# Kernel tuning notes

Measured on AMD Instinct MI355X. Metric: run time of the kernel, lower is better.

The kernel has to match this reference:

```python
import jax, jax.numpy as jnp
import numpy as np

N_ENTITIES = 200000
N_EDGES = 1200000
N_RELATIONS = 32
LATDIM = 64
N_HOPS = 2
RES_LAMBDA = 0.5  # args.res_lambda
LEAKY_SLOPE = 0.2
EPS = 1e-12


def setup_inputs() -> dict:
    key = jax.random.key(0)
    k1, k2, k3, k4, k5 = jax.random.split(key, 5)
    entity_emb = jax.random.normal(k1, (N_ENTITIES, LATDIM), dtype=jnp.float32)
    relation_emb = jax.random.normal(k2, (N_RELATIONS, LATDIM), dtype=jnp.float32)
    W = jax.random.normal(k3, (2 * LATDIM, LATDIM), dtype=jnp.float32) * (1.0 / np.sqrt(2 * LATDIM))
    edge_index = jax.random.randint(k4, (2, N_EDGES), 0, N_ENTITIES, dtype=jnp.int64)
    edge_type = jax.random.randint(k5, (N_EDGES,), 0, N_RELATIONS, dtype=jnp.int64)
    return {"entity_emb": entity_emb, "relation_emb": relation_emb, "W": W,
            "edge_index": edge_index, "edge_type": edge_type}


def _l2_normalize(x):
    # F.normalize(x) : row-wise L2 normalize with eps clamp
    n = jnp.sqrt(jnp.sum(x * x, axis=-1, keepdims=True))
    return x / jnp.maximum(n, EPS)


def _agg(entity_emb, relation_emb, W, head, tail, edge_type):
    n = entity_emb.shape[0]
    # gather head/tail embeddings -> [E, 2*D]
    a_input = jnp.concatenate([entity_emb[head], entity_emb[tail]], axis=-1)
    # attention logit per edge: ((a_input @ W) * r_e).sum(-1)
    e = jnp.sum((a_input @ W) * relation_emb[edge_type], axis=-1)
    e = jax.nn.leaky_relu(e, LEAKY_SLOPE)
    # scatter_softmax over edges grouped by head node
    m = jax.ops.segment_max(e, head, num_segments=n)
    ex = jnp.exp(e - m[head])
    denom = jax.ops.segment_sum(ex, head, num_segments=n)
    alpha = ex / denom[head]
    # scatter_sum of alpha-weighted tail embeddings
    agg_emb = jax.ops.segment_sum(entity_emb[tail] * alpha[:, None], head, num_segments=n)
    return agg_emb + entity_emb


def reference(entity_emb, relation_emb, W, edge_index, edge_type):
    head, tail = edge_index[0], edge_index[1]
    entity_res_emb = entity_emb
    ent = entity_emb
    for _ in range(N_HOPS):
        ent = _agg(ent, relation_emb, W, head, tail, edge_type)
        ent = _l2_normalize(ent)  # mess_dropout disabled (deterministic reference)
        entity_res_emb = RES_LAMBDA * entity_res_emb + ent
    return entity_res_emb
```

## Files before the change

kernel.cpp:

```cpp
#include <hip/hip_runtime.h>
#include <hip/hip_bf16.h>


#define N_ENT  200000
#define N_EDGE 1200000
#define N_REL  32
#define DIM    64
#define LEAKY  0.2f
#define CAP    32
#define NBIN   (CAP + 1)
#define SUBH   500
#define NSUB   (N_ENT / SUBH)
#define SQCAP  3500
#define I4PB   2048
#define NRB    ((N_EDGE / 4 + I4PB - 1) / I4PB)

template <int CTRL>
__device__ __forceinline__ float dpp_add(float x) {
  int t = __builtin_amdgcn_update_dpp(0, __float_as_int(x), CTRL, 0xF, 0xF, true);
  return x + __int_as_float(t);
}
__device__ __forceinline__ float red16(float x) {
  x = dpp_add<0xB1>(x);
  x = dpp_add<0x4E>(x);
  x = dpp_add<0x124>(x);
  x = dpp_add<0x128>(x);
  return x;
}

__device__ __forceinline__ float4 unpack4(uint2 u) {
  float4 t;
  t.x = __uint_as_float(u.x << 16);
  t.y = __uint_as_float(u.x & 0xFFFF0000u);
  t.z = __uint_as_float(u.y << 16);
  t.w = __uint_as_float(u.y & 0xFFFF0000u);
  return t;
}
__device__ __forceinline__ unsigned pk(float a, float b) {
  unsigned ua = __float_as_uint(a);
  ua += 0x7FFFu + ((ua >> 16) & 1u);
  unsigned ub = __float_as_uint(b);
  ub += 0x7FFFu + ((ub >> 16) & 1u);
  return (ua >> 16) | (ub & 0xFFFF0000u);
}

__global__ void prep(const float* __restrict__ W, const float* __restrict__ R,
                     float* __restrict__ Q,
                     const float4* __restrict__ ent04,
                     uint2* __restrict__ ent0b,
                     int* __restrict__ sqcnt) {
  int i = blockIdx.x * blockDim.x + threadIdx.x;
  if (i < N_REL * 2 * DIM) {
    int r = i >> 7;
    int k = i & 127;
    float acc = 0.f;
#pragma unroll 8
    for (int j = 0; j < DIM; ++j)
      acc += W[k * DIM + j] * R[r * DIM + j];
    Q[i] = acc;
  }
  if (i < NSUB) sqcnt[i] = 0;
  if (i < N_ENT * DIM / 4) {
    float4 v = ent04[i];
    ent0b[i] = make_uint2(pk(v.x, v.y), pk(v.z, v.w));
  }
}

__global__ __launch_bounds__(256) void route400(
    const int4* __restrict__ head4,
    const int4* __restrict__ tail4,
    const int4* __restrict__ type4,
    int* __restrict__ sqcnt,
    uint2* __restrict__ sqdata) {
  __shared__ int lcnt[NSUB];
  __shared__ int lbase[NSUB];
  __shared__ int lrank[NSUB];
  for (int i = threadIdx.x; i < NSUB; i += blockDim.x) {
    lcnt[i] = 0;
    lrank[i] = 0;
  }
  __syncthreads();
  int base = blockIdx.x * I4PB;
  int lim = min(N_EDGE / 4, base + I4PB);
  for (int k = base + threadIdx.x; k < lim; k += blockDim.x) {
    int4 h = head4[k];
    atomicAdd(&lcnt[h.x / SUBH], 1);
    atomicAdd(&lcnt[h.y / SUBH], 1);
    atomicAdd(&lcnt[h.z / SUBH], 1);
    atomicAdd(&lcnt[h.w / SUBH], 1);
  }
  __syncthreads();
  for (int i = threadIdx.x; i < NSUB; i += blockDim.x)
    if (lcnt[i] > 0) lbase[i] = atomicAdd(&sqcnt[i], lcnt[i]);
  __syncthreads();
  for (int k = base + threadIdx.x; k < lim; k += blockDim.x) {
    int4 h = head4[k];
    int4 t = tail4[k];
    int4 r = type4[k];
    int s, p;
    s = h.x / SUBH; p = lbase[s] + atomicAdd(&lrank[s], 1);
    if (p < SQCAP) sqdata[(size_t)s * SQCAP + p] =
        make_uint2((unsigned)t.x | ((unsigned)r.x << 18), (unsigned)h.x);
    s = h.y / SUBH; p = lbase[s] + atomicAdd(&lrank[s], 1);
    if (p < SQCAP) sqdata[(size_t)s * SQCAP + p] =
        make_uint2((unsigned)t.y | ((unsigned)r.y << 18), (unsigned)h.y);
    s = h.z / SUBH; p = lbase[s] + atomicAdd(&lrank[s], 1);
    if (p < SQCAP) sqdata[(size_t)s * SQCAP + p] =
        make_uint2((unsigned)t.z | ((unsigned)r.z << 18), (unsigned)h.z);
    s = h.w / SUBH; p = lbase[s] + atomicAdd(&lrank[s], 1);
    if (p < SQCAP) sqdata[(size_t)s * SQCAP + p] =
        make_uint2((unsigned)t.w | ((unsigned)r.w << 18), (unsigned)h.w);
  }
}

__global__ __launch_bounds__(256) void fill3s(
    const int* __restrict__ sqcnt,
    const uint2* __restrict__ sqdata,
    unsigned* __restrict__ bucket,
    unsigned* __restrict__ order) {
  __shared__ unsigned lbucket[SUBH * CAP];
  __shared__ int lcur[SUBH];
  __shared__ int lbin[NBIN];
  __shared__ int lbs[NBIN];
  __shared__ int lrk[NBIN];
  int g = blockIdx.x;
  int hbase = g * SUBH;
  for (int i = threadIdx.x; i < SUBH; i += blockDim.x) lcur[i] = 0;
  if (threadIdx.x < NBIN) { lbin[threadIdx.x] = 0; lrk[threadIdx.x] = 0; }
  __syncthreads();
  int n = min(sqcnt[g], SQCAP);
  const uint2* q = sqdata + (size_t)g * SQCAP;
  for (int k = threadIdx.x; k < n; k += blockDim.x) {
    uint2 rec = q[k];
    int lh = (int)rec.y - hbase;
    int p = atomicAdd(&lcur[lh], 1);
    if (p < CAP) lbucket[lh * CAP + p] = rec.x;
  }
  __syncthreads();
  const uint4* lb4 = (const uint4*)lbucket;
  uint4* gb4 = (uint4*)(bucket + (size_t)hbase * CAP);
  for (int i = threadIdx.x; i < SUBH * CAP / 4; i += blockDim.x) gb4[i] = lb4[i];
  for (int i = threadIdx.x; i < SUBH; i += blockDim.x)
    atomicAdd(&lbin[min(lcur[i], CAP)], 1);
  __syncthreads();
  if (threadIdx.x == 0) {
    int s = 0;
    for (int b = 0; b < NBIN; ++b) { lbs[b] = s; s += lbin[b]; }
  }
  __syncthreads();
  for (int i = threadIdx.x; i < SUBH; i += blockDim.x) {
    int d = min(lcur[i], CAP);
    int slot = lbs[d] + atomicAdd(&lrk[d], 1);
    order[(size_t)slot * NSUB + g] = (unsigned)(hbase + i) | ((unsigned)d << 18);
  }
}

template <int HOP>
__global__ __launch_bounds__(256, 8) void hop_kernel(
    const ushort* __restrict__ entb,
    const ushort* __restrict__ e0b,
    const float4* __restrict__ Qg,
    const unsigned* __restrict__ order,
    const unsigned* __restrict__ bucket,
    uint2* __restrict__ outb,
    float* __restrict__ outf) {
  __shared__ float4 sQ[N_REL * 32];
  for (int i = threadIdx.x; i < N_REL * 32; i += blockDim.x) sQ[i] = Qg[i];
  __syncthreads();
  const int lane = threadIdx.x & 63;
  const int sub = lane & 15;
  const int grp = lane >> 4;
  const int wave = (blockIdx.x * blockDim.x + threadIdx.x) >> 6;
  const int nWaves = (gridDim.x * blockDim.x) >> 6;
  const uint2* gtab = (const uint2*)entb;
  for (int n4 = wave * 4; n4 < N_ENT; n4 += nWaves * 4) {
    unsigned oe = order[n4 + grp];
    int n = (int)(oe & 0x3FFFFu);
    int len = (int)(oe >> 18);
    float4 eh = unpack4(gtab[(size_t)n * 16 + sub]);
    int b = n * CAP;
    float l = 0.f;
    float4 acc = make_float4(0.f, 0.f, 0.f, 0.f);
    unsigned p0 = 0u, p1 = 0u;
    uint2 t0 = make_uint2(0u, 0u), t1 = t0;
    if (0 < len) { p0 = bucket[b];     t0 = gtab[(size_t)(p0 & 0x3FFFFu) * 16 + sub]; }
    if (1 < len) { p1 = bucket[b + 1]; t1 = gtab[(size_t)(p1 & 0x3FFFFu) * 16 + sub]; }
    for (int i = 0; __any(i < len); ++i) {
      unsigned p2 = 0u;
      uint2 t2 = make_uint2(0u, 0u);
      if (i + 2 < len) { p2 = bucket[b + i + 2];
                         t2 = gtab[(size_t)(p2 & 0x3FFFFu) * 16 + sub]; }
      if (i < len) {
        int r = (int)(p0 >> 18);
        float4 qh = sQ[r * 32 + sub];
        float4 qt = sQ[r * 32 + 16 + sub];
        float4 et = unpack4(t0);
        float d = eh.x * qh.x + eh.y * qh.y + eh.z * qh.z + eh.w * qh.w
                + et.x * qt.x + et.y * qt.y + et.z * qt.z + et.w * qt.w;
        d = red16(d);
        float v = d > 0.f ? d : LEAKY * d;
        float ex = __expf(v);
        l += ex;
        acc.x = fmaf(ex, et.x, acc.x);
        acc.y = fmaf(ex, et.y, acc.y);
        acc.z = fmaf(ex, et.z, acc.z);
        acc.w = fmaf(ex, et.w, acc.w);
      }
      p0 = p1; t0 = t1; p1 = p2; t1 = t2;
    }
    float inv = (l > 0.f) ? 1.f / l : 0.f;
    float4 v;
    v.x = fmaf(acc.x, inv, eh.x);
    v.y = fmaf(acc.y, inv, eh.y);
    v.z = fmaf(acc.z, inv, eh.z);
    v.w = fmaf(acc.w, inv, eh.w);
    float s = v.x * v.x + v.y * v.y + v.z * v.z + v.w * v.w;
    s = red16(s);
    float rn = 1.f / fmaxf(sqrtf(s), 1e-12f);
    if (HOP == 1) {
      outb[(size_t)n * 16 + sub] = make_uint2(pk(v.x * rn, v.y * rn),
                                              pk(v.z * rn, v.w * rn));
    } else {
      float4 e0 = unpack4(((const uint2*)e0b)[(size_t)n * 16 + sub]);
      float4 o;
      o.x = fmaf(0.25f, e0.x, fmaf(0.5f, eh.x, v.x * rn));
      o.y = fmaf(0.25f, e0.y, fmaf(0.5f, eh.y, v.y * rn));
      o.z = fmaf(0.25f, e0.z, fmaf(0.5f, eh.z, v.z * rn));
      o.w = fmaf(0.25f, e0.w, fmaf(0.5f, eh.w, v.w * rn));
      ((float4*)(outf + (size_t)n * DIM))[sub] = o;
    }
  }
}

extern "C" void kernel_launch(void* const* d_in, const int* in_sizes, int n_in,
                              void* d_out, int out_size, void* d_ws, size_t ws_size,
                              hipStream_t stream) {
  const float* ent0 = (const float*)d_in[0];
  const float* rel  = (const float*)d_in[1];
  const float* W    = (const float*)d_in[2];
  const int* edge_index = (const int*)d_in[3];
  const int* etype      = (const int*)d_in[4];
  const int* head = edge_index;
  const int* tail = edge_index + N_EDGE;
  float* out = (float*)d_out;

  char* ws = (char*)d_ws;
  float*    Q      = (float*)ws;
  unsigned* bucket = (unsigned*)(ws + 16384);
  ushort*   ent0b  = (ushort*)(ws + 16384 + 25600000);
  ushort*   h1b    = (ushort*)(ws + 16384 + 51200000);
  unsigned* order  = (unsigned*)(ws + 16384 + 76800000);
  int*      sqcnt  = (int*)(ws + 16384 + 77600000);
  uint2*    sqdata = (uint2*)h1b;

  prep<<<(N_ENT * DIM / 4 + 255) / 256, 256, 0, stream>>>(
      W, rel, Q, (const float4*)ent0, (uint2*)ent0b, sqcnt);
  route400<<<NRB, 256, 0, stream>>>(
      (const int4*)head, (const int4*)tail, (const int4*)etype, sqcnt, sqdata);
  fill3s<<<NSUB, 256, 0, stream>>>(sqcnt, sqdata, bucket, order);
  hop_kernel<1><<<2048, 256, 0, stream>>>(ent0b, nullptr, (const float4*)Q,
                                          order, bucket, (uint2*)h1b, nullptr);
  hop_kernel<2><<<2048, 256, 0, stream>>>(h1b, ent0b, (const float4*)Q,
                                          order, bucket, nullptr, out);
}
```

Baseline: 235.9 us.

## Process eight nodes per wave with 8-lane groups and 16-byte gathers

Each wave now handles eight head nodes instead of four. Each node gets 8 lanes, and each lane holds 8 bf16 features loaded with a single uint4 load instead of a uint2. The cross-lane reduction drops from four DPP steps to three. The intent is fewer, wider memory transactions and more independent gather chains in flight per wave. The cost is twice the registers per lane for accumulators and tiles, and more lane divergence, since eight edge lists of different lengths now share one loop bound.

```diff
diff --git a/kernel.cpp b/kernel.cpp
--- a/kernel.cpp
+++ b/kernel.cpp
@@ -20,11 +20,10 @@
   int t = __builtin_amdgcn_update_dpp(0, __float_as_int(x), CTRL, 0xF, 0xF, true);
   return x + __int_as_float(t);
 }
-__device__ __forceinline__ float red16(float x) {
+__device__ __forceinline__ float red8(float x) {
   x = dpp_add<0xB1>(x);
   x = dpp_add<0x4E>(x);
-  x = dpp_add<0x124>(x);
-  x = dpp_add<0x128>(x);
+  x = dpp_add<0x141>(x);
   return x;
 }
 
@@ -168,66 +167,96 @@
   for (int i = threadIdx.x; i < N_REL * 32; i += blockDim.x) sQ[i] = Qg[i];
   __syncthreads();
   const int lane = threadIdx.x & 63;
-  const int sub = lane & 15;
-  const int grp = lane >> 4;
+  const int sub = lane & 7;
+  const int grp = lane >> 3;
   const int wave = (blockIdx.x * blockDim.x + threadIdx.x) >> 6;
   const int nWaves = (gridDim.x * blockDim.x) >> 6;
-  const uint2* gtab = (const uint2*)entb;
-  for (int n4 = wave * 4; n4 < N_ENT; n4 += nWaves * 4) {
-    unsigned oe = order[n4 + grp];
+  const uint4* gt4 = (const uint4*)entb;
+  for (int n8 = wave * 8; n8 < N_ENT; n8 += nWaves * 8) {
+    unsigned oe = order[n8 + grp];
     int n = (int)(oe & 0x3FFFFu);
     int len = (int)(oe >> 18);
-    float4 eh = unpack4(gtab[(size_t)n * 16 + sub]);
+    uint4 ehu = gt4[(size_t)n * 8 + sub];
+    float4 ehA = unpack4(make_uint2(ehu.x, ehu.y));
+    float4 ehB = unpack4(make_uint2(ehu.z, ehu.w));
     int b = n * CAP;
     float l = 0.f;
-    float4 acc = make_float4(0.f, 0.f, 0.f, 0.f);
+    float4 accA = make_float4(0.f, 0.f, 0.f, 0.f);
+    float4 accB = make_float4(0.f, 0.f, 0.f, 0.f);
     unsigned p0 = 0u, p1 = 0u;
-    uint2 t0 = make_uint2(0u, 0u), t1 = t0;
-    if (0 < len) { p0 = bucket[b];     t0 = gtab[(size_t)(p0 & 0x3FFFFu) * 16 + sub]; }
-    if (1 < len) { p1 = bucket[b + 1]; t1 = gtab[(size_t)(p1 & 0x3FFFFu) * 16 + sub]; }
+    uint4 t0 = make_uint4(0u, 0u, 0u, 0u), t1 = t0;
+    if (0 < len) { p0 = bucket[b];     t0 = gt4[(size_t)(p0 & 0x3FFFFu) * 8 + sub]; }
+    if (1 < len) { p1 = bucket[b + 1]; t1 = gt4[(size_t)(p1 & 0x3FFFFu) * 8 + sub]; }
     for (int i = 0; __any(i < len); ++i) {
       unsigned p2 = 0u;
-      uint2 t2 = make_uint2(0u, 0u);
+      uint4 t2 = make_uint4(0u, 0u, 0u, 0u);
       if (i + 2 < len) { p2 = bucket[b + i + 2];
-                         t2 = gtab[(size_t)(p2 & 0x3FFFFu) * 16 + sub]; }
+                         t2 = gt4[(size_t)(p2 & 0x3FFFFu) * 8 + sub]; }
       if (i < len) {
         int r = (int)(p0 >> 18);
-        float4 qh = sQ[r * 32 + sub];
-        float4 qt = sQ[r * 32 + 16 + sub];
-        float4 et = unpack4(t0);
-        float d = eh.x * qh.x + eh.y * qh.y + eh.z * qh.z + eh.w * qh.w
-                + et.x * qt.x + et.y * qt.y + et.z * qt.z + et.w * qt.w;
-        d = red16(d);
+        const float4* qr = &sQ[r * 32];
+        float4 qhA = qr[2 * sub];
+        float4 qhB = qr[2 * sub + 1];
+        float4 qtA = qr[16 + 2 * sub];
+        float4 qtB = qr[16 + 2 * sub + 1];
+        float4 etA = unpack4(make_uint2(t0.x, t0.y));
+        float4 etB = unpack4(make_uint2(t0.z, t0.w));
+        float d = ehA.x * qhA.x + ehA.y * qhA.y + ehA.z * qhA.z + ehA.w * qhA.w
+                + ehB.x * qhB.x + ehB.y * qhB.y + ehB.z * qhB.z + ehB.w * qhB.w
+                + etA.x * qtA.x + etA.y * qtA.y + etA.z * qtA.z + etA.w * qtA.w
+                + etB.x * qtB.x + etB.y * qtB.y + etB.z * qtB.z + etB.w * qtB.w;
+        d = red8(d);
         float v = d > 0.f ? d : LEAKY * d;
         float ex = __expf(v);
         l += ex;
-        acc.x = fmaf(ex, et.x, acc.x);
-        acc.y = fmaf(ex, et.y, acc.y);
-        acc.z = fmaf(ex, et.z, acc.z);
-        acc.w = fmaf(ex, et.w, acc.w);
+        accA.x = fmaf(ex, etA.x, accA.x);
+        accA.y = fmaf(ex, etA.y, accA.y);
+        accA.z = fmaf(ex, etA.z, accA.z);
+        accA.w = fmaf(ex, etA.w, accA.w);
+        accB.x = fmaf(ex, etB.x, accB.x);
+        accB.y = fmaf(ex, etB.y, accB.y);
+        accB.z = fmaf(ex, etB.z, accB.z);
+        accB.w = fmaf(ex, etB.w, accB.w);
       }
       p0 = p1; t0 = t1; p1 = p2; t1 = t2;
     }
     float inv = (l > 0.f) ? 1.f / l : 0.f;
-    float4 v;
-    v.x = fmaf(acc.x, inv, eh.x);
-    v.y = fmaf(acc.y, inv, eh.y);
-    v.z = fmaf(acc.z, inv, eh.z);
-    v.w = fmaf(acc.w, inv, eh.w);
-    float s = v.x * v.x + v.y * v.y + v.z * v.z + v.w * v.w;
-    s = red16(s);
+    float4 vA, vB;
+    vA.x = fmaf(accA.x, inv, ehA.x);
+    vA.y = fmaf(accA.y, inv, ehA.y);
+    vA.z = fmaf(accA.z, inv, ehA.z);
+    vA.w = fmaf(accA.w, inv, ehA.w);
+    vB.x = fmaf(accB.x, inv, ehB.x);
+    vB.y = fmaf(accB.y, inv, ehB.y);
+    vB.z = fmaf(accB.z, inv, ehB.z);
+    vB.w = fmaf(accB.w, inv, ehB.w);
+    float s = vA.x * vA.x + vA.y * vA.y + vA.z * vA.z + vA.w * vA.w
+            + vB.x * vB.x + vB.y * vB.y + vB.z * vB.z + vB.w * vB.w;
+    s = red8(s);
     float rn = 1.f / fmaxf(sqrtf(s), 1e-12f);
     if (HOP == 1) {
-      outb[(size_t)n * 16 + sub] = make_uint2(pk(v.x * rn, v.y * rn),
-                                              pk(v.z * rn, v.w * rn));
+      uint4 w;
+      w.x = pk(vA.x * rn, vA.y * rn);
+      w.y = pk(vA.z * rn, vA.w * rn);
+      w.z = pk(vB.x * rn, vB.y * rn);
+      w.w = pk(vB.z * rn, vB.w * rn);
+      ((uint4*)outb)[(size_t)n * 8 + sub] = w;
     } else {
-      float4 e0 = unpack4(((const uint2*)e0b)[(size_t)n * 16 + sub]);
-      float4 o;
-      o.x = fmaf(0.25f, e0.x, fmaf(0.5f, eh.x, v.x * rn));
-      o.y = fmaf(0.25f, e0.y, fmaf(0.5f, eh.y, v.y * rn));
-      o.z = fmaf(0.25f, e0.z, fmaf(0.5f, eh.z, v.z * rn));
-      o.w = fmaf(0.25f, e0.w, fmaf(0.5f, eh.w, v.w * rn));
-      ((float4*)(outf + (size_t)n * DIM))[sub] = o;
+      uint4 e0u = ((const uint4*)e0b)[(size_t)n * 8 + sub];
+      float4 e0A = unpack4(make_uint2(e0u.x, e0u.y));
+      float4 e0B = unpack4(make_uint2(e0u.z, e0u.w));
+      float4 oA, oB;
+      oA.x = fmaf(0.25f, e0A.x, fmaf(0.5f, ehA.x, vA.x * rn));
+      oA.y = fmaf(0.25f, e0A.y, fmaf(0.5f, ehA.y, vA.y * rn));
+      oA.z = fmaf(0.25f, e0A.z, fmaf(0.5f, ehA.z, vA.z * rn));
+      oA.w = fmaf(0.25f, e0A.w, fmaf(0.5f, ehA.w, vA.w * rn));
+      oB.x = fmaf(0.25f, e0B.x, fmaf(0.5f, ehB.x, vB.x * rn));
+      oB.y = fmaf(0.25f, e0B.y, fmaf(0.5f, ehB.y, vB.y * rn));
+      oB.z = fmaf(0.25f, e0B.z, fmaf(0.5f, ehB.z, vB.z * rn));
+      oB.w = fmaf(0.25f, e0B.w, fmaf(0.5f, ehB.w, vB.w * rn));
+      float4* orow = (float4*)(outf + (size_t)n * DIM);
+      orow[2 * sub] = oA;
+      orow[2 * sub + 1] = oB;
     }
   }
 }
```

New measurement: 230.1 us. 1.03x faster.
